# Performance work log

Measured on AMD Instinct MI355X. Metric: run time of the kernel, lower is better.

The kernel has to match this reference:

```python
import jax, jax.numpy as jnp
import numpy as np

NUM_USERS, NUM_ITEMS, D = 100000, 200000, 128
B, LLEN, SLEN = 4096, 200, 50
NEG = -1e9


def setup_inputs() -> dict:
    key = jax.random.key(0)
    ks = jax.random.split(key, 10)
    w_range = float(np.sqrt(3.0 / D))
    return {
        "user_table": 0.01 * jax.random.normal(ks[0], (NUM_USERS, D), dtype=jnp.float32),
        "item_table": 0.01 * jax.random.normal(ks[1], (NUM_ITEMS, D), dtype=jnp.float32),
        "W1": jax.random.uniform(ks[2], (2 * D, 16), minval=-w_range, maxval=w_range, dtype=jnp.float32),
        "b1": jnp.zeros((16,), dtype=jnp.float32),
        "W2": jax.random.uniform(ks[3], (16, 1), minval=-w_range, maxval=w_range, dtype=jnp.float32),
        "b2": jnp.zeros((1,), dtype=jnp.float32),
        "user_inputs": jax.random.randint(ks[4], (B,), 0, NUM_USERS, dtype=jnp.int64) if jax.config.jax_enable_x64 else jax.random.randint(ks[4], (B,), 0, NUM_USERS, dtype=jnp.int32),
        "L_inputs": jax.random.randint(ks[5], (B, LLEN), 0, NUM_ITEMS, dtype=jnp.int32),
        "S_inputs": jax.random.randint(ks[6], (B, SLEN), 0, NUM_ITEMS, dtype=jnp.int32),
        "item_inputs": jax.random.randint(ks[7], (B,), 0, NUM_ITEMS, dtype=jnp.int32),
    }


def reference(user_table, item_table, W1, b1, W2, b2,
              user_inputs, L_inputs, S_inputs, item_inputs):
    def att_logits(x):  # x: [..., 2D] -> [...]
        h = jax.nn.relu(x @ W1 + b1)
        return (h @ W2 + b2)[..., 0]

    def masked_softmax(logits, mask):  # softmax over last axis restricted to mask
        logits = jnp.where(mask, logits, NEG)
        return jax.nn.softmax(logits, axis=-1)

    u_emb = user_table[user_inputs]                      # [B, D]

    # ---- long-term attention over L history ----
    L_mask = L_inputs >= 0                               # [B, L]
    L_idx = jnp.where(L_mask, L_inputs, 0)
    L_emb = item_table[L_idx]                            # [B, L, D]
    uL = jnp.concatenate([jnp.broadcast_to(u_emb[:, None, :], L_emb.shape), L_emb], axis=-1)  # [B, L, 2D]
    w1 = masked_softmax(att_logits(uL), L_mask)          # [B, L]
    u_long = jnp.einsum('bl,bld->bd', w1, L_emb)         # [B, D]

    # ---- short-term attention over [u_long] + S (L assumed nonempty) ----
    S_mask = S_inputs >= 0                               # [B, S]
    S_idx = jnp.where(S_mask, S_inputs, 0)
    S_emb = item_table[S_idx]                            # [B, S, D]
    seq = jnp.concatenate([u_long[:, None, :], S_emb], axis=1)   # [B, 1+S, D]
    seq_mask = jnp.concatenate([jnp.ones((seq.shape[0], 1), dtype=bool), S_mask], axis=1)
    uSeq = jnp.concatenate([jnp.broadcast_to(u_emb[:, None, :], seq.shape), seq], axis=-1)  # [B, 1+S, 2D]
    w2 = masked_softmax(att_logits(uSeq), seq_mask)      # [B, 1+S]
    user_hybrid = jnp.einsum('bs,bsd->bd', w2, seq)      # [B, D]

    # ---- score: bmm([B,1,D], [B,D,1]) -> [B,1,1] ----
    item_emb = item_table[item_inputs]                   # [B, D]
    score = jnp.sum(user_hybrid * item_emb, axis=-1)[:, None, None]
    return score
```

## Files before the change

kernel.cpp:

```cpp
#include <hip/hip_runtime.h>
#include <math.h>
#include <stdint.h>

#define D 128
#define LLEN 200
#define SLEN 50
#define CH 50
#define TROWS 51

typedef __attribute__((ext_vector_type(8))) short short8;
typedef __attribute__((ext_vector_type(4))) float f32x4;
typedef __attribute__((address_space(3))) unsigned int lds_uint;
typedef __attribute__((address_space(1))) unsigned int gbl_uint;

__device__ __forceinline__ unsigned short f2bf(float f) {
  unsigned int u = __float_as_uint(f);
  return (unsigned short)((u + 0x7FFFu + ((u >> 16) & 1u)) >> 16);
}

__device__ __forceinline__ float wave_red_sum(float v) {
#pragma unroll
  for (int m = 32; m >= 1; m >>= 1) v += __shfl_xor(v, m, 64);
  return v;
}
__device__ __forceinline__ float block_sum(float v, float* red) {
  v = wave_red_sum(v);
  if ((threadIdx.x & 63) == 0) red[threadIdx.x >> 6] = v;
  __syncthreads();
  v = red[0] + red[1] + red[2] + red[3];
  __syncthreads();
  return v;
}

#define STAGE(ROWARR, RBASE, IT, ROFF)                                        \
  do {                                                                        \
    const int s_ = tid + (IT) * 256;                                          \
    const int rr_ = (s_ >> 5) + (ROFF);                                       \
    int gid_ = ROWARR[(RBASE) + (s_ >> 5)];                                   \
    if (gid_ < 0) gid_ = 0;                                                   \
    const float4* src_ = &it4[(size_t)gid_ * 32 + ((s_ & 31) ^ (rr_ & 7))];   \
    __builtin_amdgcn_global_load_lds(                                         \
        (const gbl_uint*)(uintptr_t)src_,                                     \
        (lds_uint*)(uintptr_t)(&ebuf[((tid & 192) + (IT) * 256) * 4 +         \
                                     (ROFF) * 128]),                          \
        16, 0, 0);                                                            \
  } while (0)

#define STAGE_CHUNK(RB)                                                \
  do {                                                                 \
    STAGE(rows1, RB, 0, 0); STAGE(rows1, RB, 1, 0);                    \
    STAGE(rows1, RB, 2, 0); STAGE(rows1, RB, 3, 0);                    \
    STAGE(rows1, RB, 4, 0); STAGE(rows1, RB, 5, 0);                    \
    if (tid < 64) STAGE(rows1, RB, 6, 0);                              \
  } while (0)

#define FMA4(WL, P, ACC)                \
  do {                                  \
    ACC.x = fmaf((WL), P.x, ACC.x);     \
    ACC.y = fmaf((WL), P.y, ACC.y);     \
    ACC.z = fmaf((WL), P.z, ACC.z);     \
  } while (0);                          \
  ACC.w = fmaf((WL), P.w, ACC.w)

template <int MODE>
__device__ __forceinline__ void mfma_logits(
    const float* eb, const unsigned short* w1t,
    int w, int lane, float upart_j, float w2j, float b2v,
    const int* rowm, int nvalid, float* w_sh, float& pacc) {
  const int jj = lane & 15, ko = lane >> 4;
  const int x = lane & 7;
  const int q0 = (2 * ko) ^ x, q1 = q0 ^ 1;
  const int row = 16 * w + jj;
  const int rowc = (row <= 50) ? row : 50;
  const float4* rp = reinterpret_cast<const float4*>(&eb[rowc * 128]);
  const unsigned short* wp = &w1t[jj * 136 + 8 * ko];
  f32x4 acc = {0.f, 0.f, 0.f, 0.f};
#pragma unroll 1
  for (int s = 0; s < 4; ++s) {
    float4 fa = rp[q0 + 8 * s];
    float4 fb = rp[q1 + 8 * s];
    short8 bfrag = *reinterpret_cast<const short8*>(wp + 32 * s);
    short8 afrag;
    afrag[0] = (short)f2bf(fa.x); afrag[1] = (short)f2bf(fa.y);
    afrag[2] = (short)f2bf(fa.z); afrag[3] = (short)f2bf(fa.w);
    afrag[4] = (short)f2bf(fb.x); afrag[5] = (short)f2bf(fb.y);
    afrag[6] = (short)f2bf(fb.z); afrag[7] = (short)f2bf(fb.w);
    acc = __builtin_amdgcn_mfma_f32_16x16x32_bf16(afrag, bfrag, acc, 0, 0, 0);
  }
  float v0 = fmaxf(upart_j + acc[0], 0.f) * w2j;
  float v1 = fmaxf(upart_j + acc[1], 0.f) * w2j;
  float v2 = fmaxf(upart_j + acc[2], 0.f) * w2j;
  float v3 = fmaxf(upart_j + acc[3], 0.f) * w2j;
#pragma unroll
  for (int m = 1; m <= 8; m <<= 1) {
    v0 += __shfl_xor(v0, m, 64);
    v1 += __shfl_xor(v1, m, 64);
    v2 += __shfl_xor(v2, m, 64);
    v3 += __shfl_xor(v3, m, 64);
  }
  if ((lane & 15) == 0) {
    const int it0 = 16 * w + 4 * (lane >> 4);
    float p0, p1, p2, p3;
    if (MODE == 0) {
      p0 = (it0 + 0 < nvalid && rowm[it0 + 0] >= 0) ? expf(v0 + b2v) : 0.f;
      p1 = (it0 + 1 < nvalid && rowm[it0 + 1] >= 0) ? expf(v1 + b2v) : 0.f;
      p2 = (it0 + 2 < nvalid && rowm[it0 + 2] >= 0) ? expf(v2 + b2v) : 0.f;
      p3 = (it0 + 3 < nvalid && rowm[it0 + 3] >= 0) ? expf(v3 + b2v) : 0.f;
    } else {
      p0 = (it0 == 0) ? expf(v0 + b2v)
                      : ((it0 < nvalid && rowm[it0 - 1] >= 0) ? expf(v0 + b2v) : 0.f);
      p1 = (it0 + 1 < nvalid && rowm[it0 + 0] >= 0) ? expf(v1 + b2v) : 0.f;
      p2 = (it0 + 2 < nvalid && rowm[it0 + 1] >= 0) ? expf(v2 + b2v) : 0.f;
      p3 = (it0 + 3 < nvalid && rowm[it0 + 2] >= 0) ? expf(v3 + b2v) : 0.f;
    }
    float4 pv;
    pv.x = p0; pv.y = p1; pv.z = p2; pv.w = p3;
    reinterpret_cast<float4*>(w_sh)[it0 >> 2] = pv;
    pacc += p0 + p1 + p2 + p3;
  }
}

__global__ void __launch_bounds__(256, 5) din_kernel(
    const float* __restrict__ user_table, const float* __restrict__ item_table,
    const float* __restrict__ W1, const float* __restrict__ b1,
    const float* __restrict__ W2, const float* __restrict__ b2,
    const int* __restrict__ user_inputs, const int* __restrict__ L_inputs,
    const int* __restrict__ S_inputs, const int* __restrict__ item_inputs,
    float* __restrict__ out) {
  __shared__ __align__(16) float ebuf[TROWS * 128];
  __shared__ __align__(16) unsigned short w1t_sh[16 * 136];
  __shared__ __align__(16) float w_sh[64];
  __shared__ int rows1[LLEN];
  __shared__ int rowsS[SLEN];
  __shared__ float upart_sh[16];
  __shared__ float red_sh[4];

  const int b = blockIdx.x;
  const int tid = threadIdx.x;
  const int lane = tid & 63;
  const int w = __builtin_amdgcn_readfirstlane(tid >> 6);
  const int col4 = tid & 31;
  const int grp = tid >> 5;
  const float4* it4 = reinterpret_cast<const float4*>(item_table);
  float* scr = &ebuf[0];

  const int urow = user_inputs[b];
  const float item_f =
      (tid < D) ? item_table[(size_t)item_inputs[b] * D + tid] : 0.f;
  if (tid < LLEN) rows1[tid] = L_inputs[(size_t)b * LLEN + tid];
  if (tid < SLEN) rowsS[tid] = S_inputs[(size_t)b * SLEN + tid];
  __syncthreads();

  STAGE_CHUNK(0);

  {
    const int j = tid & 15, g = tid >> 4;
    const float* up = &user_table[(size_t)urow * D + 8 * g];
    const float* wp = &W1[(size_t)(8 * g) * 16 + j];
    float p = 0.f;
#pragma unroll
    for (int t = 0; t < 8; ++t) p = fmaf(up[t], wp[t * 16], p);
    p += __shfl_xor(p, 16, 64);
    p += __shfl_xor(p, 32, 64);
    if (lane < 16) w_sh[w * 16 + lane] = p;
  }
#pragma unroll
  for (int i = 0; i < 8; ++i) {
    int idx = tid + i * 256;
    int j = idx & 15, k = idx >> 4;
    w1t_sh[j * 136 + k] = f2bf(W1[(size_t)(128 + k) * 16 + j]);
  }
  __syncthreads();
  if (tid < 16)
    upart_sh[tid] = b1[tid] + w_sh[tid] + w_sh[16 + tid] + w_sh[32 + tid] +
                    w_sh[48 + tid];
  __syncthreads();

  const float b2v = b2[0];
  const float upart_j = upart_sh[lane & 15];
  const float w2j = W2[lane & 15];

  float pacc = 0.f;
  float4 uacc = make_float4(0.f, 0.f, 0.f, 0.f);

#pragma unroll 1
  for (int c = 0; c < 4; ++c) {
    mfma_logits<0>(ebuf, w1t_sh, w, lane, upart_j, w2j, b2v,
                   rows1 + c * CH, CH, w_sh, pacc);
    __syncthreads();
#pragma unroll
    for (int i = 0; i < 6; ++i) {
      int l = grp + 8 * i;
      float wl = w_sh[l];
      const float4 e = reinterpret_cast<const float4*>(&ebuf[l * 128])[col4 ^ grp];
      FMA4(wl, e, uacc);
    }
    if (grp < 2) {
      int l = 48 + grp;
      float wl = w_sh[l];
      const float4 e = reinterpret_cast<const float4*>(&ebuf[l * 128])[col4 ^ grp];
      FMA4(wl, e, uacc);
    }
    if (c < 3) {
      __syncthreads();
      STAGE_CHUNK((c + 1) * CH);
      __syncthreads();
    }
  }

  const float invS1 = 1.f / block_sum(pacc, red_sh);
  uacc.x += __shfl_xor(uacc.x, 32, 64);
  uacc.y += __shfl_xor(uacc.y, 32, 64);
  uacc.z += __shfl_xor(uacc.z, 32, 64);
  uacc.w += __shfl_xor(uacc.w, 32, 64);
  if (lane < 32) reinterpret_cast<float4*>(scr)[(w << 5) + lane] = uacc;
  __syncthreads();
  float ulv = 0.f;
  if (tid < D)
    ulv = (scr[tid] + scr[128 + tid] + scr[256 + tid] + scr[384 + tid]) * invS1;
  __syncthreads();
  if (tid < D) ebuf[tid] = ulv;
  STAGE(rowsS, 0, 0, 1); STAGE(rowsS, 0, 1, 1); STAGE(rowsS, 0, 2, 1);
  STAGE(rowsS, 0, 3, 1); STAGE(rowsS, 0, 4, 1); STAGE(rowsS, 0, 5, 1);
  if (tid < 64) STAGE(rowsS, 0, 6, 1);
  __syncthreads();

  float pacc2 = 0.f;
  mfma_logits<1>(ebuf, w1t_sh, w, lane, upart_j, w2j, b2v,
                 rowsS, 51, w_sh, pacc2);
  const float invS2 = 1.f / block_sum(pacc2, red_sh);

  float4 uacc2 = make_float4(0.f, 0.f, 0.f, 0.f);
#pragma unroll
  for (int i = 0; i < 6; ++i) {
    int l = grp + 8 * i;
    float wl = w_sh[l];
    const float4 e = reinterpret_cast<const float4*>(&ebuf[l * 128])[col4 ^ grp];
    FMA4(wl, e, uacc2);
  }
  if (grp < 3) {
    int l = 48 + grp;
    float wl = w_sh[l];
    const float4 e = reinterpret_cast<const float4*>(&ebuf[l * 128])[col4 ^ grp];
    FMA4(wl, e, uacc2);
  }

  uacc2.x += __shfl_xor(uacc2.x, 32, 64);
  uacc2.y += __shfl_xor(uacc2.y, 32, 64);
  uacc2.z += __shfl_xor(uacc2.z, 32, 64);
  uacc2.w += __shfl_xor(uacc2.w, 32, 64);
  __syncthreads();
  if (lane < 32) reinterpret_cast<float4*>(scr)[(w << 5) + lane] = uacc2;
  __syncthreads();

  float sv = 0.f;
  if (tid < D) {
    float s = scr[tid] + scr[128 + tid] + scr[256 + tid] + scr[384 + tid];
    sv = s * invS2 * item_f;
  }
  float tot = block_sum(sv, red_sh);
  if (tid == 0) out[b] = tot;
}

extern "C" void kernel_launch(void* const* d_in, const int* in_sizes, int n_in,
                              void* d_out, int out_size, void* d_ws, size_t ws_size,
                              hipStream_t stream) {
  const float* user_table = (const float*)d_in[0];
  const float* item_table = (const float*)d_in[1];
  const float* W1 = (const float*)d_in[2];
  const float* b1 = (const float*)d_in[3];
  const float* W2 = (const float*)d_in[4];
  const float* b2 = (const float*)d_in[5];
  const int* user_inputs = (const int*)d_in[6];
  const int* L_inputs = (const int*)d_in[7];
  const int* S_inputs = (const int*)d_in[8];
  const int* item_inputs = (const int*)d_in[9];
  float* out = (float*)d_out;

  const int B = in_sizes[6];
  din_kernel<<<B, 256, 0, stream>>>(user_table, item_table, W1, b1, W2, b2,
                                    user_inputs, L_inputs, S_inputs, item_inputs,
                                    out);
}
```

Measured before the change: 248.5 us.

## Prefetch next chunk's embedding rows into registers while computing current chunk

Replaces the direct global-to-LDS async loads with register-staged gathers. The loads for the next 50-row chunk (and the S rows after the last L chunk) are issued before the current chunk's MFMA logits and weighted-sum work, then written to LDS afterwards. The aim is to overlap gather latency with compute instead of stalling on a synchronous stage between chunks. The cost is 7 float4 registers per thread, which may lower occupancy, plus an extra LDS write pass through VGPRs.

```diff
diff --git a/kernel.cpp b/kernel.cpp
--- a/kernel.cpp
+++ b/kernel.cpp
@@ -1,6 +1,5 @@
 #include <hip/hip_runtime.h>
 #include <math.h>
-#include <stdint.h>
 
 #define D 128
 #define LLEN 200
@@ -10,8 +9,6 @@
 
 typedef __attribute__((ext_vector_type(8))) short short8;
 typedef __attribute__((ext_vector_type(4))) float f32x4;
-typedef __attribute__((address_space(3))) unsigned int lds_uint;
-typedef __attribute__((address_space(1))) unsigned int gbl_uint;
 
 __device__ __forceinline__ unsigned short f2bf(float f) {
   unsigned int u = __float_as_uint(f);
@@ -32,26 +29,37 @@
   return v;
 }
 
-#define STAGE(ROWARR, RBASE, IT, ROFF)                                        \
-  do {                                                                        \
-    const int s_ = tid + (IT) * 256;                                          \
-    const int rr_ = (s_ >> 5) + (ROFF);                                       \
-    int gid_ = ROWARR[(RBASE) + (s_ >> 5)];                                   \
-    if (gid_ < 0) gid_ = 0;                                                   \
-    const float4* src_ = &it4[(size_t)gid_ * 32 + ((s_ & 31) ^ (rr_ & 7))];   \
-    __builtin_amdgcn_global_load_lds(                                         \
-        (const gbl_uint*)(uintptr_t)src_,                                     \
-        (lds_uint*)(uintptr_t)(&ebuf[((tid & 192) + (IT) * 256) * 4 +         \
-                                     (ROFF) * 128]),                          \
-        16, 0, 0);                                                            \
-  } while (0)
-
-#define STAGE_CHUNK(RB)                                                \
-  do {                                                                 \
-    STAGE(rows1, RB, 0, 0); STAGE(rows1, RB, 1, 0);                    \
-    STAGE(rows1, RB, 2, 0); STAGE(rows1, RB, 3, 0);                    \
-    STAGE(rows1, RB, 4, 0); STAGE(rows1, RB, 5, 0);                    \
-    if (tid < 64) STAGE(rows1, RB, 6, 0);                              \
+#define GATHER(P, ROWARR, RBASE, IT)                   \
+  do {                                                 \
+    int s_ = tid + (IT) * 256;                         \
+    if (s_ > 1599) s_ = 1599;                          \
+    int gid_ = (ROWARR)[(RBASE) + (s_ >> 5)];          \
+    if (gid_ < 0) gid_ = 0;                            \
+    P = it4[(size_t)gid_ * 32 + (s_ & 31)];            \
+  } while (0)
+
+#define GATHER7(ROWARR, RBASE)                                     \
+  do {                                                             \
+    GATHER(P0, ROWARR, RBASE, 0); GATHER(P1, ROWARR, RBASE, 1);    \
+    GATHER(P2, ROWARR, RBASE, 2); GATHER(P3, ROWARR, RBASE, 3);    \
+    GATHER(P4, ROWARR, RBASE, 4); GATHER(P5, ROWARR, RBASE, 5);    \
+    GATHER(P6, ROWARR, RBASE, 6);                                  \
+  } while (0)
+
+#define WSLOT(P, IT, ROFF)                                                  \
+  do {                                                                      \
+    int s_ = tid + (IT) * 256;                                              \
+    if (s_ < 1600) {                                                        \
+      int r_ = (s_ >> 5) + (ROFF);                                          \
+      reinterpret_cast<float4*>(&ebuf[r_ * 128])[(s_ & 31) ^ (r_ & 7)] = P; \
+    }                                                                       \
+  } while (0)
+
+#define WRITE7(ROFF)                                            \
+  do {                                                          \
+    WSLOT(P0, 0, ROFF); WSLOT(P1, 1, ROFF); WSLOT(P2, 2, ROFF); \
+    WSLOT(P3, 3, ROFF); WSLOT(P4, 4, ROFF); WSLOT(P5, 5, ROFF); \
+    WSLOT(P6, 6, ROFF);                                         \
   } while (0)
 
 #define FMA4(WL, P, ACC)                \
@@ -151,7 +159,8 @@
   if (tid < SLEN) rowsS[tid] = S_inputs[(size_t)b * SLEN + tid];
   __syncthreads();
 
-  STAGE_CHUNK(0);
+  float4 P0, P1, P2, P3, P4, P5, P6;
+  GATHER7(rows1, 0);
 
   {
     const int j = tid & 15, g = tid >> 4;
@@ -174,6 +183,7 @@
   if (tid < 16)
     upart_sh[tid] = b1[tid] + w_sh[tid] + w_sh[16 + tid] + w_sh[32 + tid] +
                     w_sh[48 + tid];
+  WRITE7(0);
   __syncthreads();
 
   const float b2v = b2[0];
@@ -185,6 +195,8 @@
 
 #pragma unroll 1
   for (int c = 0; c < 4; ++c) {
+    if (c < 3) GATHER7(rows1, (c + 1) * CH);
+    else       GATHER7(rowsS, 0);
     mfma_logits<0>(ebuf, w1t_sh, w, lane, upart_j, w2j, b2v,
                    rows1 + c * CH, CH, w_sh, pacc);
     __syncthreads();
@@ -201,9 +213,9 @@
       const float4 e = reinterpret_cast<const float4*>(&ebuf[l * 128])[col4 ^ grp];
       FMA4(wl, e, uacc);
     }
+    __syncthreads();
     if (c < 3) {
-      __syncthreads();
-      STAGE_CHUNK((c + 1) * CH);
+      WRITE7(0);
       __syncthreads();
     }
   }
@@ -220,9 +232,7 @@
     ulv = (scr[tid] + scr[128 + tid] + scr[256 + tid] + scr[384 + tid]) * invS1;
   __syncthreads();
   if (tid < D) ebuf[tid] = ulv;
-  STAGE(rowsS, 0, 0, 1); STAGE(rowsS, 0, 1, 1); STAGE(rowsS, 0, 2, 1);
-  STAGE(rowsS, 0, 3, 1); STAGE(rowsS, 0, 4, 1); STAGE(rowsS, 0, 5, 1);
-  if (tid < 64) STAGE(rowsS, 0, 6, 1);
+  WRITE7(1);
   __syncthreads();
 
   float pacc2 = 0.f;
```

Result: slower. 333.4 us (+34.1%).

## Give each wave its own L-history slice to drop block barriers

Applied to the files above, without the earlier changes.

Splits the long-term history across waves: each wave stages and processes its own 50 rows in 16-row sub-chunks in a private 16-row LDS region. Waits on its own vmcnt/lgkmcnt instead of block-wide __syncthreads, so waves pipeline independently. The LDS buffer grows to 64 rows and the launch-bound occupancy hint drops from 5 to 4. The short-term weighted sum is moved before the block reduction and one barrier is removed, which risks LDS race subtleties and lower occupancy.

```diff
diff --git a/kernel.cpp b/kernel.cpp
--- a/kernel.cpp
+++ b/kernel.cpp
@@ -5,8 +5,6 @@
 #define D 128
 #define LLEN 200
 #define SLEN 50
-#define CH 50
-#define TROWS 51
 
 typedef __attribute__((ext_vector_type(8))) short short8;
 typedef __attribute__((ext_vector_type(4))) float f32x4;
@@ -32,26 +30,37 @@
   return v;
 }
 
-#define STAGE(ROWARR, RBASE, IT, ROFF)                                        \
-  do {                                                                        \
-    const int s_ = tid + (IT) * 256;                                          \
-    const int rr_ = (s_ >> 5) + (ROFF);                                       \
-    int gid_ = ROWARR[(RBASE) + (s_ >> 5)];                                   \
-    if (gid_ < 0) gid_ = 0;                                                   \
-    const float4* src_ = &it4[(size_t)gid_ * 32 + ((s_ & 31) ^ (rr_ & 7))];   \
-    __builtin_amdgcn_global_load_lds(                                         \
-        (const gbl_uint*)(uintptr_t)src_,                                     \
-        (lds_uint*)(uintptr_t)(&ebuf[((tid & 192) + (IT) * 256) * 4 +         \
-                                     (ROFF) * 128]),                          \
-        16, 0, 0);                                                            \
+#define STAGEW(IT, LBASE)                                                   \
+  do {                                                                      \
+    const int t_ = lane + (IT) * 64;                                        \
+    const int rl_ = t_ >> 5;                                                \
+    int gid_ = rows1[(LBASE) + rl_];                                        \
+    if (gid_ < 0) gid_ = 0;                                                 \
+    const float4* src_ =                                                    \
+        &it4[(size_t)gid_ * 32 + ((t_ & 31) ^ ((R0 + rl_) & 7))];           \
+    __builtin_amdgcn_global_load_lds(                                       \
+        (const gbl_uint*)(uintptr_t)src_,                                   \
+        (lds_uint*)(uintptr_t)(&ebuf[R0 * 128 + (IT) * 256]), 16, 0, 0);    \
   } while (0)
 
-#define STAGE_CHUNK(RB)                                                \
-  do {                                                                 \
-    STAGE(rows1, RB, 0, 0); STAGE(rows1, RB, 1, 0);                    \
-    STAGE(rows1, RB, 2, 0); STAGE(rows1, RB, 3, 0);                    \
-    STAGE(rows1, RB, 4, 0); STAGE(rows1, RB, 5, 0);                    \
-    if (tid < 64) STAGE(rows1, RB, 6, 0);                              \
+#define STAGEW8(LBASE)                                        \
+  do {                                                        \
+    STAGEW(0, LBASE); STAGEW(1, LBASE); STAGEW(2, LBASE);     \
+    STAGEW(3, LBASE); STAGEW(4, LBASE); STAGEW(5, LBASE);     \
+    STAGEW(6, LBASE); STAGEW(7, LBASE);                       \
+  } while (0)
+
+#define STAGE_S(IT)                                                          \
+  do {                                                                       \
+    const int s_ = tid + (IT) * 256;                                         \
+    const int rr_ = (s_ >> 5) + 1;                                           \
+    int gid_ = rowsS[s_ >> 5];                                               \
+    if (gid_ < 0) gid_ = 0;                                                  \
+    const float4* src_ = &it4[(size_t)gid_ * 32 + ((s_ & 31) ^ (rr_ & 7))];  \
+    __builtin_amdgcn_global_load_lds(                                        \
+        (const gbl_uint*)(uintptr_t)src_,                                    \
+        (lds_uint*)(uintptr_t)(&ebuf[((tid & 192) + (IT) * 256) * 4 + 128]), \
+        16, 0, 0);                                                           \
   } while (0)
 
 #define FMA4(WL, P, ACC)                \
@@ -68,10 +77,10 @@
     int w, int lane, float upart_j, float w2j, float b2v,
     const int* rowm, int nvalid, float* w_sh, float& pacc) {
   const int jj = lane & 15, ko = lane >> 4;
-  const int x = lane & 7;
+  const int row = 16 * w + jj;
+  const int rowc = (MODE == 1 && row > 50) ? 50 : row;
+  const int x = rowc & 7;
   const int q0 = (2 * ko) ^ x, q1 = q0 ^ 1;
-  const int row = 16 * w + jj;
-  const int rowc = (row <= 50) ? row : 50;
   const float4* rp = reinterpret_cast<const float4*>(&eb[rowc * 128]);
   const unsigned short* wp = &w1t[jj * 136 + 8 * ko];
   f32x4 acc = {0.f, 0.f, 0.f, 0.f};
@@ -120,14 +129,14 @@
   }
 }
 
-__global__ void __launch_bounds__(256, 5) din_kernel(
+__global__ void __launch_bounds__(256, 4) din_kernel(
     const float* __restrict__ user_table, const float* __restrict__ item_table,
     const float* __restrict__ W1, const float* __restrict__ b1,
     const float* __restrict__ W2, const float* __restrict__ b2,
     const int* __restrict__ user_inputs, const int* __restrict__ L_inputs,
     const int* __restrict__ S_inputs, const int* __restrict__ item_inputs,
     float* __restrict__ out) {
-  __shared__ __align__(16) float ebuf[TROWS * 128];
+  __shared__ __align__(16) float ebuf[64 * 128];
   __shared__ __align__(16) unsigned short w1t_sh[16 * 136];
   __shared__ __align__(16) float w_sh[64];
   __shared__ int rows1[LLEN];
@@ -139,8 +148,9 @@
   const int tid = threadIdx.x;
   const int lane = tid & 63;
   const int w = __builtin_amdgcn_readfirstlane(tid >> 6);
-  const int col4 = tid & 31;
-  const int grp = tid >> 5;
+  const int R0 = 16 * w;
+  const int par = lane >> 5;
+  const int c32 = lane & 31;
   const float4* it4 = reinterpret_cast<const float4*>(item_table);
   float* scr = &ebuf[0];
 
@@ -151,7 +161,7 @@
   if (tid < SLEN) rowsS[tid] = S_inputs[(size_t)b * SLEN + tid];
   __syncthreads();
 
-  STAGE_CHUNK(0);
+  STAGEW8(50 * w);
 
   {
     const int j = tid & 15, g = tid >> 4;
@@ -184,27 +194,28 @@
   float4 uacc = make_float4(0.f, 0.f, 0.f, 0.f);
 
 #pragma unroll 1
-  for (int c = 0; c < 4; ++c) {
+  for (int s = 0; s < 4; ++s) {
+    const int cs = (s < 3) ? 16 : 2;
+    asm volatile("s_waitcnt vmcnt(0)" ::: "memory");
+    __builtin_amdgcn_sched_barrier(0);
     mfma_logits<0>(ebuf, w1t_sh, w, lane, upart_j, w2j, b2v,
-                   rows1 + c * CH, CH, w_sh, pacc);
-    __syncthreads();
-#pragma unroll
-    for (int i = 0; i < 6; ++i) {
-      int l = grp + 8 * i;
-      float wl = w_sh[l];
-      const float4 e = reinterpret_cast<const float4*>(&ebuf[l * 128])[col4 ^ grp];
-      FMA4(wl, e, uacc);
-    }
-    if (grp < 2) {
-      int l = 48 + grp;
-      float wl = w_sh[l];
-      const float4 e = reinterpret_cast<const float4*>(&ebuf[l * 128])[col4 ^ grp];
-      FMA4(wl, e, uacc);
-    }
-    if (c < 3) {
-      __syncthreads();
-      STAGE_CHUNK((c + 1) * CH);
-      __syncthreads();
+                   rows1 + 34 * w + 16 * s, R0 + cs, w_sh, pacc);
+#pragma unroll
+    for (int i = 0; i < 8; ++i) {
+      if (par + 2 * i < cs) {
+        const int l = R0 + par + 2 * i;
+        float wl = w_sh[l];
+        const float4 e =
+            reinterpret_cast<const float4*>(&ebuf[l * 128])[c32 ^ (l & 7)];
+        FMA4(wl, e, uacc);
+      }
+    }
+    if (s < 3) {
+      asm volatile("s_waitcnt lgkmcnt(0)" ::: "memory");
+      __builtin_amdgcn_sched_barrier(0);
+      const int nb = 50 * w + 16 * (s + 1);
+      if (s < 2) STAGEW8(nb);
+      else       STAGEW(0, nb);
     }
   }
 
@@ -220,36 +231,29 @@
     ulv = (scr[tid] + scr[128 + tid] + scr[256 + tid] + scr[384 + tid]) * invS1;
   __syncthreads();
   if (tid < D) ebuf[tid] = ulv;
-  STAGE(rowsS, 0, 0, 1); STAGE(rowsS, 0, 1, 1); STAGE(rowsS, 0, 2, 1);
-  STAGE(rowsS, 0, 3, 1); STAGE(rowsS, 0, 4, 1); STAGE(rowsS, 0, 5, 1);
-  if (tid < 64) STAGE(rowsS, 0, 6, 1);
+  STAGE_S(0); STAGE_S(1); STAGE_S(2); STAGE_S(3); STAGE_S(4); STAGE_S(5);
+  if (tid < 64) STAGE_S(6);
   __syncthreads();
 
   float pacc2 = 0.f;
   mfma_logits<1>(ebuf, w1t_sh, w, lane, upart_j, w2j, b2v,
                  rowsS, 51, w_sh, pacc2);
+  float4 uacc2 = make_float4(0.f, 0.f, 0.f, 0.f);
+#pragma unroll
+  for (int i = 0; i < 8; ++i) {
+    const int l = R0 + par + 2 * i;
+    if (l < 51) {
+      float wl = w_sh[l];
+      const float4 e =
+          reinterpret_cast<const float4*>(&ebuf[l * 128])[c32 ^ (l & 7)];
+      FMA4(wl, e, uacc2);
+    }
+  }
   const float invS2 = 1.f / block_sum(pacc2, red_sh);
-
-  float4 uacc2 = make_float4(0.f, 0.f, 0.f, 0.f);
-#pragma unroll
-  for (int i = 0; i < 6; ++i) {
-    int l = grp + 8 * i;
-    float wl = w_sh[l];
-    const float4 e = reinterpret_cast<const float4*>(&ebuf[l * 128])[col4 ^ grp];
-    FMA4(wl, e, uacc2);
-  }
-  if (grp < 3) {
-    int l = 48 + grp;
-    float wl = w_sh[l];
-    const float4 e = reinterpret_cast<const float4*>(&ebuf[l * 128])[col4 ^ grp];
-    FMA4(wl, e, uacc2);
-  }
-
   uacc2.x += __shfl_xor(uacc2.x, 32, 64);
   uacc2.y += __shfl_xor(uacc2.y, 32, 64);
   uacc2.z += __shfl_xor(uacc2.z, 32, 64);
   uacc2.w += __shfl_xor(uacc2.w, 32, 64);
-  __syncthreads();
   if (lane < 32) reinterpret_cast<float4*>(scr)[(w << 5) + lane] = uacc2;
   __syncthreads();
 
```

After: 250.2 us. No clear change (+0.7%).
